# Kernel optimization log

Measured on AMD Instinct MI355X. Metric: run time of the kernel, lower is better.

## Reference

```python
import jax, jax.numpy as jnp
import numpy as np

T, G, D = 64, 1024, 128      # timesteps, detections per timestep, feature dim
N = T * G                    # total points; output rows = 3 + D = 131 cols


def setup_inputs() -> dict:
    key = jax.random.key(0)
    k1, k2 = jax.random.split(key)
    # time column: T distinct timestamps, G detections each (already time-sorted)
    times = jnp.repeat(jnp.arange(T, dtype=jnp.float32), G)
    xy = jax.random.uniform(k1, (N, 2), dtype=jnp.float32) * 128.0
    coor = jnp.concatenate([times[:, None], xy], axis=1)          # [N, 3]
    features = jax.random.normal(k2, (N, D), dtype=jnp.float32)   # [N, 128]
    return {"coor": coor, "features": features, "min_length": 8}


def _traverse(nxt):
    """Greedy chain building with a visited set (faithful to the torch loop).
    nxt[i] = precomputed best cosine match of point i in the next time group
    (-1 if i is in the last group). Returns (out_nodes, cid, clen):
      out_nodes[p] = node emitted at output slot p (all N slots filled),
      cid[p]       = chain id of slot p,
      clen[c]      = length of chain c.
    """
    def chain_cond(carry):
        visited, out, cid, p, cur, length, c = carry
        nx = nxt[cur]
        return (nx >= 0) & (~visited[nx])

    def chain_body(carry):
        visited, out, cid, p, cur, length, c = carry
        nx = nxt[cur]
        visited = visited.at[nx].set(True)
        out = out.at[p].set(nx)
        cid = cid.at[p].set(c)
        return (visited, out, cid, p + 1, nx, length + 1, c)

    def start_chain(st, start):
        visited, out, cid, clen, p, c = st
        visited = visited.at[start].set(True)
        out = out.at[p].set(start)
        cid = cid.at[p].set(c)
        carry = (visited, out, cid, p + 1, start, jnp.int32(1), c)
        visited, out, cid, p, cur, length, _ = jax.lax.while_loop(
            chain_cond, chain_body, carry)
        clen = clen.at[c].set(length)
        return (visited, out, cid, clen, p, c + 1)

    def body(start, st):
        start = jnp.int32(start)
        return jax.lax.cond(st[0][start], lambda s: s,
                            lambda s: start_chain(s, start), st)

    init = (jnp.zeros(N, bool),
            jnp.full(N, -1, jnp.int32),
            jnp.zeros(N, jnp.int32),
            jnp.zeros(N, jnp.int32),
            jnp.int32(0), jnp.int32(0))
    visited, out, cid, clen, p, c = jax.lax.fori_loop(0, N, body, init)
    return out, cid, clen


def reference(coor, features, min_length):
    # sort all points by time (stable; input is already time-sorted)
    order = jnp.argsort(coor[:, 0], stable=True)
    coor = coor[order]
    features = features[order]

    # --- vectorized precompute of the greedy next-match graph ---
    # group points by timestamp: [T, G, D]
    f = features.reshape(T, G, D)
    fn = f / jnp.maximum(jnp.linalg.norm(f, axis=-1, keepdims=True), 1e-6)
    # cosine sims between each time group and the next one: [T-1, G, G]
    sims = jnp.einsum('tgd,thd->tgh', fn[:-1], fn[1:])
    best = jnp.argmax(sims, axis=-1).astype(jnp.int32)        # [T-1, G]
    nxt = jnp.concatenate([
        (jnp.arange(1, T, dtype=jnp.int32)[:, None] * G + best).reshape(-1),
        jnp.full((G,), -1, jnp.int32)])                        # [N]
    nxt = jax.lax.stop_gradient(nxt)

    # --- sequential greedy traversal with visited set ---
    out_nodes, cid, clen = _traverse(nxt)

    # rows = [coor || features] in trajectory order
    rows = jnp.concatenate([coor, features], axis=1)[out_nodes]  # [N, 3+D]
    keep = clen[cid] >= min_length
    # pack kept rows to the top (order preserved), zero-pad the rest
    perm = jnp.argsort(~keep, stable=True)
    return jnp.where(keep[perm][:, None], rows[perm], 0.0)       # [N, 131]
```

## Files before the change

### kernel.cpp

```cpp
#include <hip/hip_runtime.h>
#include <hip/hip_bf16.h>
#include <hip/hip_fp16.h>

#define TT 64
#define GN 1024
#define DK 128
#define NN (TT * GN)
#define OUTC 131
#define TAU 5e-3f

typedef _Float16 f16x8 __attribute__((ext_vector_type(8)));
typedef float    f32x4 __attribute__((ext_vector_type(4)));

__device__ __forceinline__ unsigned f2h(float f) {
    return (unsigned)__half_as_ushort(__float2half(f));
}

__device__ __forceinline__ unsigned hup(float x) {
    __half h = __float2half(x);
    unsigned short b = __half_as_ushort(h);
    if (__half2float(h) < x)
        b = (b & 0x8000) ? (unsigned short)(b - 1) : (unsigned short)(b + 1);
    return (unsigned)b;
}

__device__ __forceinline__ void gload_lds16(const void* g, void* l) {
    __builtin_amdgcn_global_load_lds(
        (const __attribute__((address_space(1))) unsigned int*)g,
        (__attribute__((address_space(3))) unsigned int*)l, 16, 0, 0);
}

__global__ void kconv(const float* __restrict__ feat, unsigned* __restrict__ fh,
                      float* __restrict__ rnf, double* __restrict__ rnd,
                      int* __restrict__ rcnt, int* __restrict__ clen) {
    if (blockIdx.x == 0 && threadIdx.x < 63) rcnt[threadIdx.x] = 0;
    if (blockIdx.x < 256) clen[blockIdx.x * 256 + threadIdx.x] = 0;
    int row  = blockIdx.x * 4 + (threadIdx.x >> 6);
    int lane = threadIdx.x & 63;
    const float* fr = feat + (size_t)row * DK;
    float2 v = *(const float2*)(fr + lane * 2);
    fh[(size_t)row * 64 + lane] = f2h(v.x) | (f2h(v.y) << 16);
    double s = (double)v.x * (double)v.x + (double)v.y * (double)v.y;
    #pragma unroll
    for (int off = 32; off > 0; off >>= 1)
        s += __shfl_down(s, off);
    if (lane == 0) {
        double m = sqrt(s);
        if (m < 1e-6) m = 1e-6;
        double r = 1.0 / m;
        rnd[row] = r;
        rnf[row] = (float)r;
    }
}

__global__ __launch_bounds__(512) void ksim(const unsigned* __restrict__ fh,
                                            const float* __restrict__ rnf,
                                            unsigned short* __restrict__ nxt16,
                                            int* __restrict__ rcnt,
                                            int* __restrict__ rlistT,
                                            uint2* __restrict__ skt) {
    __shared__ int Tiles[2][8192];

    int id = blockIdx.x;
    int t  = id >> 3;
    int mt = id & 7;

    int tid  = threadIdx.x;
    int wave = tid >> 6;
    int lane = tid & 63;
    int la = lane & 15;
    int lq = lane >> 4;
    int wr = (wave & 1) * 64;
    int cg = wave >> 1;
    int wc = cg * 32;

    const int* Ag = (const int*)fh + ((size_t)t * GN + mt * 128) * 64;
    const int* Bg = (const int*)fh + (size_t)(t + 1) * GN * 64;

    #pragma unroll
    for (int i = 0; i < 4; ++i) {
        int L = i * 512 + tid;
        int row = L >> 4, colG = (L & 15) ^ (row & 7);
        gload_lds16(Bg + row * 64 + colG * 4, &Tiles[0][L * 4]);
    }

    f16x8 af[4][4];
    #pragma unroll
    for (int kc = 0; kc < 4; ++kc)
        #pragma unroll
        for (int x = 0; x < 4; ++x)
            af[kc][x] = __builtin_bit_cast(f16x8,
                *(const int4*)&Ag[(wr + x * 16 + la) * 64 + (kc * 4 + lq) * 4]);

    float t1[4], t2[4]; int i1[4];
    #pragma unroll
    for (int s = 0; s < 4; ++s) { t1[s] = -3.4e38f; t2[s] = -3.4e38f; i1[s] = 0x7fffffff; }

    const float* rB = rnf + (size_t)(t + 1) * GN;
    __syncthreads();

    #pragma unroll 2
    for (int ntb = 0; ntb < 8; ++ntb) {
        int cur = ntb & 1;
        if (ntb < 7) {
            const int* Bn = Bg + (ntb + 1) * 128 * 64;
            int* dst = Tiles[cur ^ 1];
            #pragma unroll
            for (int i = 0; i < 4; ++i) {
                int L = i * 512 + tid;
                int row = L >> 4, colG = (L & 15) ^ (row & 7);
                gload_lds16(Bn + row * 64 + colG * 4, &dst[L * 4]);
            }
        }

        f32x4 acc[4][2];
        #pragma unroll
        for (int at = 0; at < 4; ++at)
            #pragma unroll
            for (int ct = 0; ct < 2; ++ct) acc[at][ct] = (f32x4){0.f, 0.f, 0.f, 0.f};

        const int* Bt = Tiles[cur];
        #pragma unroll
        for (int kc = 0; kc < 4; ++kc) {
            int sw = ((kc * 4 + lq) ^ (la & 7)) << 2;
            f16x8 bf[2];
            #pragma unroll
            for (int x = 0; x < 2; ++x)
                bf[x] = __builtin_bit_cast(f16x8, *(const int4*)&Bt[(wc + x * 16 + la) * 64 + sw]);
            #pragma unroll
            for (int at = 0; at < 4; ++at)
                #pragma unroll
                for (int ct = 0; ct < 2; ++ct)
                    acc[at][ct] = __builtin_amdgcn_mfma_f32_16x16x32_f16(
                        bf[ct], af[kc][at], acc[at][ct], 0, 0, 0);
        }

        #pragma unroll
        for (int ct = 0; ct < 2; ++ct) {
            float4 rnv = *(const float4*)&rB[ntb * 128 + wc + ct * 16 + lq * 4];
            int nbase = ntb * 128 + wc + ct * 16 + lq * 4;
            float rn[4] = {rnv.x, rnv.y, rnv.z, rnv.w};
            #pragma unroll
            for (int at = 0; at < 4; ++at) {
                #pragma unroll
                for (int reg = 0; reg < 4; ++reg) {
                    float v = acc[at][ct][reg] * rn[reg];
                    t2[at] = fmaxf(t2[at], fminf(v, t1[at]));
                    if (v > t1[at]) { t1[at] = v; i1[at] = nbase + reg; }
                }
            }
        }
        __syncthreads();
    }

    {
        uint2* sko = skt + (size_t)(cg * 4 + lq) * (63 * GN)
                         + (size_t)t * GN + mt * 128;
        #pragma unroll
        for (int s = 0; s < 4; ++s)
            sko[wr + s * 16 + la] = make_uint2(__float_as_uint(t1[s]),
                                               (hup(t2[s]) << 16) | (unsigned)i1[s]);
    }

    #pragma unroll
    for (int m = 16; m <= 32; m <<= 1) {
        #pragma unroll
        for (int s = 0; s < 4; ++s) {
            float o1 = __shfl_xor(t1[s], m);
            float o2 = __shfl_xor(t2[s], m);
            int   oi = __shfl_xor(i1[s], m);
            bool take = (o1 > t1[s]) || (o1 == t1[s] && oi < i1[s]);
            float nt2 = take ? fmaxf(o2, t1[s]) : fmaxf(t2[s], o1);
            if (take) { t1[s] = o1; i1[s] = oi; }
            t2[s] = nt2;
        }
    }

    float* mv1 = (float*)Tiles[0];
    float* mv2 = mv1 + 512;
    int*   mi1 = (int*)(mv2 + 512);
    if (lq == 0) {
        #pragma unroll
        for (int s = 0; s < 4; ++s) {
            int idx = (wr + s * 16 + la) * 4 + cg;
            mv1[idx] = t1[s]; mv2[idx] = t2[s]; mi1[idx] = i1[s];
        }
    }
    __syncthreads();

    if (tid < 128) {
        int r4 = tid * 4;
        float best = mv1[r4], sec = mv2[r4];
        int bi = mi1[r4];
        #pragma unroll
        for (int c = 1; c < 4; ++c) {
            float v1 = mv1[r4 + c], v2 = mv2[r4 + c];
            int  ii = mi1[r4 + c];
            if (v1 > best || (v1 == best && ii < bi)) {
                sec = fmaxf(sec, fmaxf(best, v2)); best = v1; bi = ii;
            } else {
                sec = fmaxf(sec, v1);
            }
        }
        int grow = mt * 128 + tid;
        if (best - sec < TAU) {
            int p = atomicAdd(&rcnt[t], 1);
            rlistT[t * 1024 + p] = grow;
        } else {
            nxt16[t * GN + grow] = (unsigned short)bi;
        }
    }
}

__global__ __launch_bounds__(256) void krescue(const float* __restrict__ feat,
                                               const double* __restrict__ rnd,
                                               const int* __restrict__ rcnt,
                                               const int* __restrict__ rlistT,
                                               const uint2* __restrict__ skt,
                                               unsigned short* __restrict__ nxt16) {
    int bid = blockIdx.x;
    int t = bid >> 3;
    int nr = rcnt[t];
    if (nr == 0) return;
    int tid  = threadIdx.x;
    int wave = tid >> 6, lane = tid & 63;
    int wk = (bid & 7) * 4 + wave;
    int g  = lane >> 2;
    int o  = (lane & 3) * 32;

    const float*  Bt = feat + (size_t)(t + 1) * GN * DK;
    const double* rb = rnd + (size_t)(t + 1) * GN;

    for (int ri = wk; ri < nr; ri += 32) {
        int arow = rlistT[t * 1024 + ri];

        const float* ar = feat + ((size_t)t * GN + arow) * DK + o;
        double av[32];
        #pragma unroll
        for (int j = 0; j < 32; j += 4) {
            float4 a4 = *(const float4*)(ar + j);
            av[j] = a4.x; av[j + 1] = a4.y; av[j + 2] = a4.z; av[j + 3] = a4.w;
        }

        size_t gb = (size_t)t * GN + arow;
        uint2 eg = skt[(size_t)g * (63 * GN) + gb];
        float t1  = __uint_as_float(eg.x);
        float t2u = __half2float(__ushort_as_half((unsigned short)(eg.y >> 16)));
        int   ic  = (int)(eg.y & 1023u);

        float best = t1;
        best = fmaxf(best, __shfl_xor(best, 4));
        best = fmaxf(best, __shfl_xor(best, 8));
        best = fmaxf(best, __shfl_xor(best, 16));
        best = fmaxf(best, __shfl_xor(best, 32));
        float thr = best - TAU;

        double bv = -1.0e300; int bi = 0x7fffffff;

        {
            int c = (t1 >= thr) ? ic : -1;
            double d = 0.0;
            if (c >= 0) {
                const float* br = Bt + (size_t)c * DK + o;
                #pragma unroll
                for (int jj = 0; jj < 32; jj += 4) {
                    float4 b4 = *(const float4*)(br + jj);
                    d = fma(av[jj],     (double)b4.x, d);
                    d = fma(av[jj + 1], (double)b4.y, d);
                    d = fma(av[jj + 2], (double)b4.z, d);
                    d = fma(av[jj + 3], (double)b4.w, d);
                }
            }
            d += __shfl_xor(d, 1); d += __shfl_xor(d, 2);
            if (c >= 0) {
                double v = d * rb[c];
                if (v > bv || (v == bv && c < bi)) { bv = v; bi = c; }
            }
        }

        #pragma unroll 1
        for (int s = 0; s < 16; ++s) {
            float ey = __shfl(t2u, s * 4);
            if (!(ey >= thr)) continue;
            int cgs = s >> 2, lqs = s & 3;
            #pragma unroll 1
            for (int r = 0; r < 4; ++r) {
                int j = r * 16 + g;
                int c = (j >> 3) * 128 + cgs * 32 + ((j >> 2) & 1) * 16
                      + lqs * 4 + (j & 3);
                const float* br = Bt + (size_t)c * DK + o;
                double d = 0.0;
                #pragma unroll
                for (int jj = 0; jj < 32; jj += 4) {
                    float4 b4 = *(const float4*)(br + jj);
                    d = fma(av[jj],     (double)b4.x, d);
                    d = fma(av[jj + 1], (double)b4.y, d);
                    d = fma(av[jj + 2], (double)b4.z, d);
                    d = fma(av[jj + 3], (double)b4.w, d);
                }
                d += __shfl_xor(d, 1); d += __shfl_xor(d, 2);
                double v = d * rb[c];
                if (v > bv || (v == bv && c < bi)) { bv = v; bi = c; }
            }
        }

        #pragma unroll
        for (int m = 4; m <= 32; m <<= 1) {
            double ov = __shfl_xor(bv, m);
            int    oi = __shfl_xor(bi, m);
            if (ov > bv || (ov == bv && oi < bi)) { bv = ov; bi = oi; }
        }

        if (lane == 0) nxt16[t * GN + arow] = (unsigned short)bi;
    }
}

__global__ __launch_bounds__(1024) void kgraph(const unsigned short* __restrict__ nxt16,
                                               int* __restrict__ chain_of) {
    __shared__ unsigned short ns[64 * 1024];
    __shared__ int winner[2 * GN];
    int g = threadIdx.x;

    #pragma unroll
    for (int i = 0; i < 8; ++i)
        gload_lds16((const char*)nxt16 + ((size_t)i * 1024 + g) * 16,
                    (char*)ns + ((size_t)i * 1024 + g) * 16);

    winner[g] = 0x7fffffff;
    chain_of[g] = g;
    __syncthreads();

    int mychain = g;
    for (int t = 0; t < TT - 1; ++t) {
        int* Wa = winner + (t & 1) * GN;
        int* Wb = winner + ((t + 1) & 1) * GN;
        int j = ns[t * GN + g];
        atomicMin(&Wa[j], mychain);
        Wb[g] = 0x7fffffff;
        __syncthreads();
        int w = Wa[g];
        mychain = (w == 0x7fffffff) ? (((t + 1) << 10) | g) : w;
        ns[t * GN + g] = (unsigned short)mychain;
        __syncthreads();
    }

    for (int t = 0; t < TT - 1; ++t)
        chain_of[(t + 1) * GN + g] = ns[t * GN + g];
}

__global__ void kclen(const int* __restrict__ chain_of, int* __restrict__ clen) {
    int i = blockIdx.x * 256 + threadIdx.x;
    atomicAdd(&clen[chain_of[i]], 1);
}

__global__ __launch_bounds__(1024) void kseg(const int* __restrict__ chain_of,
                                             const int* __restrict__ clen,
                                             const int* __restrict__ minp,
                                             int* __restrict__ oloc,
                                             int* __restrict__ partial) {
    __shared__ int ps[1024];
    int b = blockIdx.x, tid = threadIdx.x;
    int i = b * 1024 + tid;
    int ml = *minp;
    int cl = clen[i];
    int v = (chain_of[i] == i && cl >= ml) ? cl : 0;
    ps[tid] = v;
    __syncthreads();
    for (int off = 1; off < 1024; off <<= 1) {
        int add = (tid >= off) ? ps[tid - off] : 0;
        __syncthreads();
        ps[tid] += add;
        __syncthreads();
    }
    oloc[i] = ps[tid] - v;
    if (tid == 1023) partial[b] = ps[tid];
}

__global__ __launch_bounds__(256) void kout(const float* __restrict__ coor,
                                            const float* __restrict__ feat,
                                            const int* __restrict__ chain_of,
                                            const int* __restrict__ clen,
                                            const int* __restrict__ oloc,
                                            const int* __restrict__ partial,
                                            const int* __restrict__ minp,
                                            float* __restrict__ out) {
    __shared__ int pb[64];
    __shared__ int stot;
    int tid = threadIdx.x;
    if (tid < 64) {
        int v = partial[tid];
        int acc = v;
        #pragma unroll
        for (int off = 1; off < 64; off <<= 1) {
            int o = __shfl_up(acc, off);
            if (tid >= off) acc += o;
        }
        pb[tid] = acc - v;
        if (tid == 63) stot = acc;
    }
    __syncthreads();

    int node = blockIdx.x * 4 + (tid >> 6);
    int lane = tid & 63;
    int s = chain_of[node];
    if (clen[s] >= *minp) {
        int row = oloc[s] + pb[s >> 10] + (node >> 10) - (s >> 10);
        float* orow = out + (size_t)row * OUTC;
        const float* f = feat + (size_t)node * DK;
        if (lane < 3) orow[lane] = coor[(size_t)node * 3 + lane];
        orow[3 + lane]  = f[lane];
        orow[67 + lane] = f[64 + lane];
    }

    int zrow = stot + blockIdx.x * 4 + (tid >> 6);
    if (zrow < NN) {
        float* orow = out + (size_t)zrow * OUTC;
        orow[lane] = 0.f;
        orow[64 + lane] = 0.f;
        if (lane < 3) orow[128 + lane] = 0.f;
    }
}

extern "C" void kernel_launch(void* const* d_in, const int* in_sizes, int n_in,
                              void* d_out, int out_size, void* d_ws, size_t ws_size,
                              hipStream_t stream) {
    const float* coor   = (const float*)d_in[0];
    const float* feat   = (const float*)d_in[1];
    const int*   minlen = (const int*)d_in[2];
    float*       out    = (float*)d_out;

    char* ws = (char*)d_ws;
    double*         rnd      = (double*)(ws);
    float*          rnf      = (float*)(ws + 524288);
    unsigned short* nxt16    = (unsigned short*)(ws + 786432);
    int*            chain_of = (int*)(ws + 917504);
    int*            clen     = (int*)(ws + 1179648);
    int*            oloc     = (int*)(ws + 1441792);
    int*            rcnt     = (int*)(ws + 1703936);
    int*            partial  = (int*)(ws + 1704192);
    int*            rlistT   = (int*)(ws + 1705216);
    unsigned*       fh       = (unsigned*)(ws + 2097152);
    uint2*          skt      = (uint2*)(ws + 18874368);

    kconv<<<NN / 4, 256, 0, stream>>>(feat, fh, rnf, rnd, rcnt, clen);

    ksim<<<63 * 8, 512, 0, stream>>>(fh, rnf, nxt16, rcnt, rlistT, skt);

    krescue<<<63 * 8, 256, 0, stream>>>(feat, rnd, rcnt, rlistT, skt, nxt16);

    kgraph<<<1, GN, 0, stream>>>(nxt16, chain_of);
    kclen<<<NN / 256, 256, 0, stream>>>(chain_of, clen);
    kseg<<<64, 1024, 0, stream>>>(chain_of, clen, minlen, oloc, partial);
    kout<<<NN / 4, 256, 0, stream>>>(coor, feat, chain_of, clen, oloc, partial,
                                     minlen, out);
}
```

Baseline: 197.9 us.

## Give each wave private LDS B-tile buffers and drop block-wide barriers in sim loop

The B tiles are now staged into per-wave LDS buffers. Each wave loads only the 32 columns it consumes, so two waves sharing a column group each load their own copy. The loop's __syncthreads is replaced by per-wave s_waitcnt vmcnt calls, letting waves progress independently. The reduction scratch moves to separate shared arrays. The costs are more LDS (8x16KB plus 6KB), duplicated global loads, and reliance on vmcnt counting to order the async LDS loads.

```diff
diff --git a/kernel.cpp b/kernel.cpp
--- a/kernel.cpp
+++ b/kernel.cpp
@@ -59,7 +59,10 @@
                                             int* __restrict__ rcnt,
                                             int* __restrict__ rlistT,
                                             uint2* __restrict__ skt) {
-    __shared__ int Tiles[2][8192];
+    __shared__ int Tiles[8][4096];
+    __shared__ float mv1[512];
+    __shared__ float mv2[512];
+    __shared__ int   mi1[512];
 
     int id = blockIdx.x;
     int t  = id >> 3;
@@ -76,13 +79,21 @@
 
     const int* Ag = (const int*)fh + ((size_t)t * GN + mt * 128) * 64;
     const int* Bg = (const int*)fh + (size_t)(t + 1) * GN * 64;
-
-    #pragma unroll
-    for (int i = 0; i < 4; ++i) {
-        int L = i * 512 + tid;
-        int row = L >> 4, colG = (L & 15) ^ (row & 7);
-        gload_lds16(Bg + row * 64 + colG * 4, &Tiles[0][L * 4]);
-    }
+    int* myT = &Tiles[wave][0];
+
+    #define STAGE_Q(ntb, b)                                                  \
+        {                                                                    \
+            const int* Bq = Bg + ((ntb) * 128 + cg * 32) * 64;               \
+            _Pragma("unroll")                                                \
+            for (int i = 0; i < 8; ++i) {                                    \
+                int gidx = i * 64 + lane;                                    \
+                int row = gidx >> 4, colG = (gidx & 15) ^ (row & 7);         \
+                gload_lds16(Bq + row * 64 + colG * 4,                        \
+                            myT + (b) * 2048 + gidx * 4);                    \
+            }                                                                \
+        }
+
+    STAGE_Q(0, 0)
 
     f16x8 af[4][4];
     #pragma unroll
@@ -97,20 +108,17 @@
     for (int s = 0; s < 4; ++s) { t1[s] = -3.4e38f; t2[s] = -3.4e38f; i1[s] = 0x7fffffff; }
 
     const float* rB = rnf + (size_t)(t + 1) * GN;
-    __syncthreads();
+
+    asm volatile("s_waitcnt vmcnt(0)" ::: "memory");
 
     #pragma unroll 2
     for (int ntb = 0; ntb < 8; ++ntb) {
         int cur = ntb & 1;
         if (ntb < 7) {
-            const int* Bn = Bg + (ntb + 1) * 128 * 64;
-            int* dst = Tiles[cur ^ 1];
-            #pragma unroll
-            for (int i = 0; i < 4; ++i) {
-                int L = i * 512 + tid;
-                int row = L >> 4, colG = (L & 15) ^ (row & 7);
-                gload_lds16(Bn + row * 64 + colG * 4, &dst[L * 4]);
-            }
+            STAGE_Q(ntb + 1, cur ^ 1)
+            asm volatile("s_waitcnt vmcnt(8)" ::: "memory");
+        } else {
+            asm volatile("s_waitcnt vmcnt(0)" ::: "memory");
         }
 
         f32x4 acc[4][2];
@@ -119,14 +127,14 @@
             #pragma unroll
             for (int ct = 0; ct < 2; ++ct) acc[at][ct] = (f32x4){0.f, 0.f, 0.f, 0.f};
 
-        const int* Bt = Tiles[cur];
+        const int* Bt = myT + cur * 2048;
         #pragma unroll
         for (int kc = 0; kc < 4; ++kc) {
             int sw = ((kc * 4 + lq) ^ (la & 7)) << 2;
             f16x8 bf[2];
             #pragma unroll
             for (int x = 0; x < 2; ++x)
-                bf[x] = __builtin_bit_cast(f16x8, *(const int4*)&Bt[(wc + x * 16 + la) * 64 + sw]);
+                bf[x] = __builtin_bit_cast(f16x8, *(const int4*)&Bt[(x * 16 + la) * 64 + sw]);
             #pragma unroll
             for (int at = 0; at < 4; ++at)
                 #pragma unroll
@@ -150,8 +158,8 @@
                 }
             }
         }
-        __syncthreads();
-    }
+    }
+    #undef STAGE_Q
 
     {
         uint2* sko = skt + (size_t)(cg * 4 + lq) * (63 * GN)
@@ -176,9 +184,6 @@
         }
     }
 
-    float* mv1 = (float*)Tiles[0];
-    float* mv2 = mv1 + 512;
-    int*   mi1 = (int*)(mv2 + 512);
     if (lq == 0) {
         #pragma unroll
         for (int s = 0; s < 4; ++s) {
```

After: 198.6 us. Within noise of the previous version (+0.3%).
